# Performance work log

Hardware: AMD Instinct MI355X
Metric: run time of the kernel (lower is better)

The kernel has to match this reference:

```python
import jax, jax.numpy as jnp
import numpy as np

B, C, H, W = 8, 128, 64, 64   # batch, hidden_dim, spatial
CIN = 192                      # input_dim
N, K, R, DFF = 1, 4, 8, 512    # d_state, scan dirs, dt_rank=ceil(128/16), mlp hidden
EPS = 1e-5


def _conv1x1(t, w, b=None):
    y = jnp.einsum('bchw,oc->bohw', t, w)
    return y + b[None, :, None, None] if b is not None else y


def _ln_cf(t, g, bta):
    # LayerNorm over channel dim (channel_first)
    mu = t.mean(1, keepdims=True)
    var = ((t - mu) ** 2).mean(1, keepdims=True)
    return (t - mu) * jax.lax.rsqrt(var + EPS) * g[None, :, None, None] + bta[None, :, None, None]


def _forward(h, cz, cr, cq, x,
             in_proj_w, in_proj_b, ln1_g, ln1_b,
             ssm_in_w, conv_w, conv_b,
             x_proj_w, dt_w, dt_b, A_logs, Ds,
             outnorm_g, outnorm_b, out_proj_w,
             ln2_g, ln2_b, fc1_w, fc1_b, fc2_w, fc2_b,
             gate_w, gate_b):
    combined = jnp.concatenate([h, x], axis=1)          # [B, C+CIN, H, W]
    feat = _conv1x1(combined, in_proj_w, in_proj_b)     # [B, C, H, W]

    # ---- SS2D (v2_noz, channel_first) ----
    u = _conv1x1(_ln_cf(feat, ln1_g, ln1_b), ssm_in_w)  # in_proj (no bias)
    u = jax.lax.conv_general_dilated(u, conv_w, (1, 1), [(1, 1), (1, 1)],
                                     dimension_numbers=('NCHW', 'OIHW', 'NCHW'),
                                     feature_group_count=C)
    u = jax.nn.silu(u + conv_b[None, :, None, None])

    L = H * W
    x0 = u.reshape(B, C, L)
    x1 = u.transpose(0, 1, 3, 2).reshape(B, C, L)       # column-major scan
    xs = jnp.stack([x0, x1, x0[..., ::-1], x1[..., ::-1]], axis=1)  # [B,K,C,L]

    x_dbl = jnp.einsum('bkcl,kdc->bkdl', xs, x_proj_w)  # [B,K,R+2N,L]
    dts, Bs, Cs = jnp.split(x_dbl, [R, R + N], axis=2)
    delta = jax.nn.softplus(jnp.einsum('bkrl,kcr->bkcl', dts, dt_w) + dt_b[None, :, :, None])
    A = -jnp.exp(A_logs).reshape(K, C, N)
    D = Ds.reshape(K, C)

    dA = jnp.exp(delta[..., None] * A[None, :, :, None, :])                   # [B,K,C,L,N]
    dBu = (delta * xs)[..., None] * Bs.transpose(0, 1, 3, 2)[:, :, None, :, :]  # [B,K,C,L,N]

    def step(hst, inp):
        dA_t, dBu_t, C_t = inp
        hst = dA_t * hst + dBu_t                         # [B,K,C,N]
        return hst, jnp.einsum('bkcn,bkn->bkc', hst, C_t)

    init = jnp.zeros((B, K, C, N), u.dtype)
    _, ys = jax.lax.scan(step, init,
                         (dA.transpose(3, 0, 1, 2, 4),
                          dBu.transpose(3, 0, 1, 2, 4),
                          Cs.transpose(3, 0, 1, 2)))
    ys = ys.transpose(1, 2, 3, 0)                        # [B,K,C,L]
    ys = ys + D[None, :, :, None] * xs

    # cross-merge: undo flips and transposes, sum directions
    y = ys[:, 0] + ys[:, 2, :, ::-1]
    y_t = ys[:, 1] + ys[:, 3, :, ::-1]
    y = y + y_t.reshape(B, C, W, H).transpose(0, 1, 3, 2).reshape(B, C, L)
    y = y.reshape(B, C, H, W)
    y = _ln_cf(y, outnorm_g, outnorm_b)
    ssm_out = _conv1x1(y, out_proj_w)

    # ---- VSSBlock residuals (drop_path identity in eval) ----
    z = feat + ssm_out
    m = _conv1x1(_ln_cf(z, ln2_g, ln2_b), fc1_w, fc1_b)
    m = jax.nn.gelu(m, approximate=False)
    m = _conv1x1(m, fc2_w, fc2_b)
    z = z + m

    # ---- gated update ----
    g = jax.nn.sigmoid(_conv1x1(z, gate_w, gate_b))
    return g * z + (1.0 - g) * h


def setup_inputs() -> dict:
    key = jax.random.key(0)
    ks = jax.random.split(key, 20)
    rn = lambda i, shape, s=0.02: jax.random.normal(ks[i], shape, jnp.float32) * s
    return dict(
        h=jax.random.normal(ks[0], (B, C, H, W), jnp.float32),
        cz=jax.random.normal(ks[1], (B, C, H, W), jnp.float32),
        cr=jax.random.normal(ks[2], (B, C, H, W), jnp.float32),
        cq=jax.random.normal(ks[3], (B, C, H, W), jnp.float32),
        x=jax.random.normal(ks[4], (B, CIN, H, W), jnp.float32),
        in_proj_w=rn(5, (C, C + CIN)), in_proj_b=jnp.zeros(C, jnp.float32),
        ln1_g=jnp.ones(C, jnp.float32), ln1_b=jnp.zeros(C, jnp.float32),
        ssm_in_w=rn(6, (C, C)),
        conv_w=rn(7, (C, 1, 3, 3), 0.1), conv_b=jnp.zeros(C, jnp.float32),
        x_proj_w=rn(8, (K, R + 2 * N, C)),
        dt_w=rn(9, (K, C, R), 0.1), dt_b=rn(10, (K, C), 0.1),
        A_logs=jnp.zeros((K * C, N), jnp.float32),
        Ds=jnp.ones(K * C, jnp.float32),
        outnorm_g=jnp.ones(C, jnp.float32), outnorm_b=jnp.zeros(C, jnp.float32),
        out_proj_w=rn(11, (C, C)),
        ln2_g=jnp.ones(C, jnp.float32), ln2_b=jnp.zeros(C, jnp.float32),
        fc1_w=rn(12, (DFF, C)), fc1_b=jnp.zeros(DFF, jnp.float32),
        fc2_w=rn(13, (C, DFF)), fc2_b=jnp.zeros(C, jnp.float32),
        gate_w=rn(14, (C, C)), gate_b=jnp.zeros(C, jnp.float32),
    )


def reference(h, cz, cr, cq, x,
              in_proj_w, in_proj_b, ln1_g, ln1_b,
              ssm_in_w, conv_w, conv_b,
              x_proj_w, dt_w, dt_b, A_logs, Ds,
              outnorm_g, outnorm_b, out_proj_w,
              ln2_g, ln2_b, fc1_w, fc1_b, fc2_w, fc2_b,
              gate_w, gate_b):
    return _forward(h, cz, cr, cq, x,
                    in_proj_w, in_proj_b, ln1_g, ln1_b,
                    ssm_in_w, conv_w, conv_b,
                    x_proj_w, dt_w, dt_b, A_logs, Ds,
                    outnorm_g, outnorm_b, out_proj_w,
                    ln2_g, ln2_b, fc1_w, fc1_b, fc2_w, fc2_b,
                    gate_w, gate_b)
```

## Files before the change

### kernel.cpp

```cpp
#include <hip/hip_runtime.h>
#include <hip/hip_bf16.h>

constexpr int B_ = 8, C_ = 128, Hh = 64, Ww = 64, L_ = Hh * Ww;
constexpr int CIN_ = 192, K_ = 4, Rr = 8, DFF_ = 512;
constexpr long SZ1 = (long)B_ * C_ * L_;
constexpr float EPSf = 1e-5f;
constexpr float LOG2E = 1.44269504088896f;
constexpr float LN2f  = 0.693147180559945f;

#define DEVI __device__ __forceinline__

using s16x4 = __attribute__((ext_vector_type(4))) short;
using s16x8 = __attribute__((ext_vector_type(8))) short;
using f32x4 = __attribute__((ext_vector_type(4))) float;

DEVI float sigm(float x) { return 1.f / (1.f + __expf(-x)); }
DEVI float geluf(float x) { return 0.5f * x * (1.f + erff(x * 0.70710678118654752f)); }
DEVI float siluf(float x) { return x * sigm(x); }

DEVI unsigned short f2bf(float f) {
    unsigned u = __float_as_uint(f);
    u += 0x7fffu + ((u >> 16) & 1u);
    return (unsigned short)(u >> 16);
}
DEVI float bf2f(unsigned short u) { return __uint_as_float((unsigned)u << 16); }

DEVI int tadr(int pos) { return ((pos & 63) << 6) | (pos >> 6); }

template <int BN, bool ACC, bool BIAS, bool XGELU, bool SIG, bool GATE, bool SPLIT,
          bool XLN, bool LNOUT, bool XBF, bool OUTBF>
__global__ __launch_bounds__(256) void gemm_k(
    const float* __restrict__ W, const float* __restrict__ X1, long sX1,
    const float* __restrict__ X2, long sX2, int splitRow,
    const float* __restrict__ bias,
    const float* __restrict__ xmu, const float* __restrict__ xrs,
    const float* __restrict__ xg, const float* __restrict__ xbt,
    float* __restrict__ NOut, const float* __restrict__ og, const float* __restrict__ obt,
    float* __restrict__ Cp, long sC, int M, int N, int K)
{
    constexpr int NI = BN / 32;
    __shared__ unsigned short sA[128][40];
    __shared__ unsigned short sB[BN][40];
    const int tid = threadIdx.x;
    const int bn = blockIdx.x, bm = blockIdx.y, bz = blockIdx.z;
    const float* X1b = X1 + (XBF ? 0 : (long)bz * sX1);
    const unsigned short* X1u = XBF ? ((const unsigned short*)X1 + (long)bz * sX1) : nullptr;
    const float* X2b = (SPLIT || GATE) ? (X2 + (long)bz * sX2) : nullptr;
    float* Cb = Cp + (long)bz * sC;
    unsigned short* Cu = OUTBF ? ((unsigned short*)Cp + (long)bz * sC) : nullptr;
    const int n0 = bn * BN, m0 = bm * 128;

    const int l = tid & 63, w = tid >> 6;
    const int wm = w >> 1, wn = w & 1;
    const int lr = l & 15, lk = (l >> 4) * 8;

    const int awrow = tid >> 1, awk = (tid & 1) * 16;

    f32x4 acc[4][NI];
#pragma unroll
    for (int i = 0; i < 4; i++)
#pragma unroll
        for (int j = 0; j < NI; j++) acc[i][j] = (f32x4)0.f;

    for (int k0 = 0; k0 < K; k0 += 32) {
        {
            const float* wp = W + (long)(m0 + awrow) * K + k0 + awk;
            float4 f0 = *(const float4*)(wp + 0);
            float4 f1 = *(const float4*)(wp + 4);
            float4 f2 = *(const float4*)(wp + 8);
            float4 f3 = *(const float4*)(wp + 12);
            s16x8 v0, v1;
            v0[0]=f2bf(f0.x); v0[1]=f2bf(f0.y); v0[2]=f2bf(f0.z); v0[3]=f2bf(f0.w);
            v0[4]=f2bf(f1.x); v0[5]=f2bf(f1.y); v0[6]=f2bf(f1.z); v0[7]=f2bf(f1.w);
            v1[0]=f2bf(f2.x); v1[1]=f2bf(f2.y); v1[2]=f2bf(f2.z); v1[3]=f2bf(f2.w);
            v1[4]=f2bf(f3.x); v1[5]=f2bf(f3.y); v1[6]=f2bf(f3.z); v1[7]=f2bf(f3.w);
            *(s16x8*)&sA[awrow][awk] = v0;
            *(s16x8*)&sA[awrow][awk + 8] = v1;
        }
        if constexpr (BN == 128) {
            const int bnb = tid & 31, bkb = tid >> 5;
            const int krow = k0 + bkb * 4;
            const int colk = n0 + bnb * 4;
            float4 r0, r1, r2, r3;
            if constexpr (XBF) {
                ushort4 a0 = *(const ushort4*)(X1u + (long)krow * N + colk);
                ushort4 a1 = *(const ushort4*)(X1u + (long)(krow + 1) * N + colk);
                ushort4 a2 = *(const ushort4*)(X1u + (long)(krow + 2) * N + colk);
                ushort4 a3 = *(const ushort4*)(X1u + (long)(krow + 3) * N + colk);
                r0 = make_float4(bf2f(a0.x), bf2f(a0.y), bf2f(a0.z), bf2f(a0.w));
                r1 = make_float4(bf2f(a1.x), bf2f(a1.y), bf2f(a1.z), bf2f(a1.w));
                r2 = make_float4(bf2f(a2.x), bf2f(a2.y), bf2f(a2.z), bf2f(a2.w));
                r3 = make_float4(bf2f(a3.x), bf2f(a3.y), bf2f(a3.z), bf2f(a3.w));
            } else {
                const float* xp;
                if (SPLIT && krow >= splitRow)
                    xp = X2b + (long)(krow - splitRow) * N + colk;
                else
                    xp = X1b + (long)krow * N + colk;
                r0 = *(const float4*)(xp + 0 * (long)N);
                r1 = *(const float4*)(xp + 1 * (long)N);
                r2 = *(const float4*)(xp + 2 * (long)N);
                r3 = *(const float4*)(xp + 3 * (long)N);
            }
            if (XGELU) {
                r0.x=geluf(r0.x); r0.y=geluf(r0.y); r0.z=geluf(r0.z); r0.w=geluf(r0.w);
                r1.x=geluf(r1.x); r1.y=geluf(r1.y); r1.z=geluf(r1.z); r1.w=geluf(r1.w);
                r2.x=geluf(r2.x); r2.y=geluf(r2.y); r2.z=geluf(r2.z); r2.w=geluf(r2.w);
                r3.x=geluf(r3.x); r3.y=geluf(r3.y); r3.z=geluf(r3.z); r3.w=geluf(r3.w);
            }
            const float* p0 = (const float*)&r0;
            const float* p1 = (const float*)&r1;
            const float* p2 = (const float*)&r2;
            const float* p3 = (const float*)&r3;
#pragma unroll
            for (int c = 0; c < 4; c++) {
                s16x4 v;
                v[0] = f2bf(p0[c]); v[1] = f2bf(p1[c]);
                v[2] = f2bf(p2[c]); v[3] = f2bf(p3[c]);
                *(s16x4*)&sB[bnb * 4 + c][bkb * 4] = v;
            }
        } else {
            const int bnb = tid & 15, bkb = tid >> 4;
            const int krow = k0 + bkb * 2;
            const int col0 = n0 + bnb * 4;
            float4 r0, r1;
            if constexpr (XBF) {
                ushort4 a0 = *(const ushort4*)(X1u + (long)krow * N + col0);
                ushort4 a1 = *(const ushort4*)(X1u + (long)(krow + 1) * N + col0);
                r0 = make_float4(bf2f(a0.x), bf2f(a0.y), bf2f(a0.z), bf2f(a0.w));
                r1 = make_float4(bf2f(a1.x), bf2f(a1.y), bf2f(a1.z), bf2f(a1.w));
            } else {
                const float* xpa;
                const float* xpb;
                if (SPLIT && krow >= splitRow)
                    xpa = X2b + (long)(krow - splitRow) * N + col0;
                else
                    xpa = X1b + (long)krow * N + col0;
                if (SPLIT && (krow + 1) >= splitRow)
                    xpb = X2b + (long)(krow + 1 - splitRow) * N + col0;
                else
                    xpb = X1b + (long)(krow + 1) * N + col0;
                r0 = *(const float4*)xpa;
                r1 = *(const float4*)xpb;
                if (XLN) {
                    float4 m4 = *(const float4*)(xmu + (long)bz * N + col0);
                    float4 s4 = *(const float4*)(xrs + (long)bz * N + col0);
                    float ga = xg[krow], be = xbt[krow];
                    r0.x=(r0.x-m4.x)*s4.x*ga+be; r0.y=(r0.y-m4.y)*s4.y*ga+be;
                    r0.z=(r0.z-m4.z)*s4.z*ga+be; r0.w=(r0.w-m4.w)*s4.w*ga+be;
                    ga = xg[krow + 1]; be = xbt[krow + 1];
                    r1.x=(r1.x-m4.x)*s4.x*ga+be; r1.y=(r1.y-m4.y)*s4.y*ga+be;
                    r1.z=(r1.z-m4.z)*s4.z*ga+be; r1.w=(r1.w-m4.w)*s4.w*ga+be;
                }
            }
            if (XGELU) {
                r0.x=geluf(r0.x); r0.y=geluf(r0.y); r0.z=geluf(r0.z); r0.w=geluf(r0.w);
                r1.x=geluf(r1.x); r1.y=geluf(r1.y); r1.z=geluf(r1.z); r1.w=geluf(r1.w);
            }
            const float* p0 = (const float*)&r0;
            const float* p1 = (const float*)&r1;
#pragma unroll
            for (int c = 0; c < 4; c++) {
                unsigned v = (unsigned)f2bf(p0[c]) | ((unsigned)f2bf(p1[c]) << 16);
                *(unsigned*)&sB[bnb * 4 + c][bkb * 2] = v;
            }
        }
        __syncthreads();
        s16x8 af[4], bf[NI];
#pragma unroll
        for (int mi = 0; mi < 4; mi++) af[mi] = *(const s16x8*)&sA[wm * 64 + mi * 16 + lr][lk];
#pragma unroll
        for (int ni = 0; ni < NI; ni++) bf[ni] = *(const s16x8*)&sB[wn * (BN / 2) + ni * 16 + lr][lk];
#pragma unroll
        for (int mi = 0; mi < 4; mi++)
#pragma unroll
            for (int ni = 0; ni < NI; ni++)
                acc[mi][ni] = __builtin_amdgcn_mfma_f32_16x16x32_bf16(af[mi], bf[ni], acc[mi][ni], 0, 0, 0);
        __syncthreads();
    }

    float ps[NI], pq[NI];
    if (LNOUT) {
#pragma unroll
        for (int ni = 0; ni < NI; ni++) { ps[ni] = 0.f; pq[ni] = 0.f; }
    }
#pragma unroll
    for (int mi = 0; mi < 4; mi++) {
#pragma unroll
        for (int r = 0; r < 4; r++) {
            const int row = m0 + wm * 64 + mi * 16 + (l >> 4) * 4 + r;
            const float bv = BIAS ? bias[row] : 0.f;
#pragma unroll
            for (int ni = 0; ni < NI; ni++) {
                const int col = n0 + wn * (BN / 2) + ni * 16 + lr;
                float v = acc[mi][ni][r] + bv;
                if constexpr (OUTBF) {
                    Cu[(long)row * N + col] = f2bf(v);
                } else {
                    float* cp = Cb + (long)row * N + col;
                    if (ACC) v += *cp;
                    if (SIG) v = sigm(v);
                    if (GATE) {
                        v = sigm(v);
                        float zv = X1b[(long)row * N + col];
                        float hv = X2b[(long)row * N + col];
                        v = hv + v * (zv - hv);
                    }
                    *cp = v;
                }
                if (LNOUT) {
                    acc[mi][ni][r] = v;
                    ps[ni] += v; pq[ni] += v * v;
                }
            }
        }
    }
    if constexpr (LNOUT) {
        __shared__ float redS[2][2][NI][16];
        __shared__ float redQ[2][2][NI][16];
        __shared__ float muL[BN], rsL[BN];
#pragma unroll
        for (int ni = 0; ni < NI; ni++) {
            ps[ni] += __shfl_xor(ps[ni], 16, 64);
            ps[ni] += __shfl_xor(ps[ni], 32, 64);
            pq[ni] += __shfl_xor(pq[ni], 16, 64);
            pq[ni] += __shfl_xor(pq[ni], 32, 64);
        }
        if (l < 16) {
#pragma unroll
            for (int ni = 0; ni < NI; ni++) {
                redS[wm][wn][ni][l] = ps[ni];
                redQ[wm][wn][ni][l] = pq[ni];
            }
        }
        __syncthreads();
        if (tid < BN) {
            const int cc = tid;
            const int wn2 = cc >> 5, rem = cc & 31;
            const int ni2 = rem >> 4, lr2 = rem & 15;
            float s = redS[0][wn2][ni2][lr2] + redS[1][wn2][ni2][lr2];
            float q = redQ[0][wn2][ni2][lr2] + redQ[1][wn2][ni2][lr2];
            float mu = s * (1.f / 128.f);
            float var = q * (1.f / 128.f) - mu * mu;
            muL[cc] = mu;
            rsL[cc] = rsqrtf(var + EPSf);
        }
        __syncthreads();
        unsigned short* Nb = (unsigned short*)NOut + (long)bz * sC;
#pragma unroll
        for (int mi = 0; mi < 4; mi++) {
#pragma unroll
            for (int r = 0; r < 4; r++) {
                const int row = m0 + wm * 64 + mi * 16 + (l >> 4) * 4 + r;
                const float gg = og[row], bb = obt[row];
#pragma unroll
                for (int ni = 0; ni < NI; ni++) {
                    const int cc = wn * (BN / 2) + ni * 16 + lr;
                    const int col = n0 + cc;
                    float v = acc[mi][ni][r];
                    Nb[(long)row * N + col] = f2bf((v - muL[cc]) * rsL[cc] * gg + bb);
                }
            }
        }
    }
}

__global__ __launch_bounds__(256) void ln_stats_k(const float* __restrict__ in,
                                                  float* __restrict__ mu,
                                                  float* __restrict__ rs)
{
    __shared__ float s1[4][64], s2[4][64];
    const int tid = threadIdx.x;
    const int p = tid & 63, q = tid >> 6;
    const long posg = (long)blockIdx.x * 64 + p;
    const int b = (int)(posg / L_);
    const int pp = (int)(posg % L_);
    const float* base = in + ((long)b * C_ + q * 32) * L_ + pp;
    float s = 0.f, sq = 0.f;
#pragma unroll
    for (int i = 0; i < 32; i++) {
        float t = base[(long)i * L_];
        s += t; sq += t * t;
    }
    s1[q][p] = s; s2[q][p] = sq;
    __syncthreads();
    if (q == 0) {
        float ts = s1[0][p] + s1[1][p] + s1[2][p] + s1[3][p];
        float tq = s2[0][p] + s2[1][p] + s2[2][p] + s2[3][p];
        float m = ts * (1.f / 128.f);
        float var = tq * (1.f / 128.f) - m * m;
        mu[posg] = m;
        rs[posg] = rsqrtf(var + EPSf);
    }
}

__global__ __launch_bounds__(256) void dwconvT_k(const unsigned short* __restrict__ in,
                                                 const float* __restrict__ wts,
                                                 const float* __restrict__ bias,
                                                 float* __restrict__ uo,
                                                 float* __restrict__ uTo)
{
    __shared__ float t[64][65];
    const long plane = blockIdx.x;
    const int c = (int)(plane & 127);
    const int tid = threadIdx.x;
    const unsigned short* src = in + plane * (long)L_;
#pragma unroll
    for (int ii = 0; ii < 16; ii++) {
        int idx = tid + ii * 256;
        t[idx >> 6][idx & 63] = bf2f(src[idx]);
    }
    float kw[9];
#pragma unroll
    for (int q = 0; q < 9; q++) kw[q] = wts[c * 9 + q];
    const float bc = bias[c];
    __syncthreads();
    float r[16];
#pragma unroll
    for (int ii = 0; ii < 16; ii++) {
        int idx = tid + ii * 256;
        int h = idx >> 6, w2 = idx & 63;
        float acc = bc;
#pragma unroll
        for (int dh = -1; dh <= 1; dh++) {
            int hh = h + dh;
            if ((unsigned)hh >= 64u) continue;
#pragma unroll
            for (int dw = -1; dw <= 1; dw++) {
                int ww2 = w2 + dw;
                if ((unsigned)ww2 >= 64u) continue;
                acc += t[hh][ww2] * kw[(dh + 1) * 3 + (dw + 1)];
            }
        }
        r[ii] = siluf(acc);
    }
    __syncthreads();
    float* ud = uo + plane * (long)L_;
#pragma unroll
    for (int ii = 0; ii < 16; ii++) {
        int idx = tid + ii * 256;
        t[idx >> 6][idx & 63] = r[ii];
        ud[idx] = r[ii];
    }
    __syncthreads();
    float* utd = uTo + plane * (long)L_;
#pragma unroll
    for (int ii = 0; ii < 16; ii++) {
        int idx = tid + ii * 256;
        utd[idx] = t[idx & 63][idx >> 6];
    }
}

template <bool ADD>
__global__ __launch_bounds__(256) void transp_k(const float* __restrict__ src,
                                                float* __restrict__ dst)
{
    __shared__ float t[64][65];
    const long plane = blockIdx.x;
    const float* s = src + plane * (long)L_;
    float* d = dst + plane * (long)L_;
    const int tid = threadIdx.x;
#pragma unroll
    for (int i = 0; i < 16; i++) {
        int idx = tid + i * 256;
        t[idx >> 6][idx & 63] = s[idx];
    }
    __syncthreads();
#pragma unroll
    for (int i = 0; i < 16; i++) {
        int idx = tid + i * 256;
        int r = idx >> 6, cc = idx & 63;
        float val = t[cc][r];
        if (ADD) d[idx] += val; else d[idx] = val;
    }
}

__global__ __launch_bounds__(256) void xdbl2_k(const float* __restrict__ u,
                                               const float* __restrict__ uT,
                                               const float* __restrict__ xw,
                                               float* __restrict__ out)
{
    __shared__ float wsm[2][16][132];
    const int pair = blockIdx.y, b = blockIdx.z;
    const int tid = threadIdx.x;
#pragma unroll
    for (int i = 0; i < 8; i++) {
        int idx = tid * 8 + i;
        wsm[0][idx >> 7][idx & 127] = xw[pair * 2048 + idx];
        wsm[1][idx >> 7][idx & 127] = xw[(pair + 2) * 2048 + idx];
    }
    __syncthreads();
    const int dg = (tid & 3) * 4;
    const int lo = tid >> 2;
    const int pos = blockIdx.x * 64 + lo;
    const float* usrc = (pair ? uT : u) + (long)b * C_ * L_ + pos;
    float a0[4] = {0.f, 0.f, 0.f, 0.f};
    float a1[4] = {0.f, 0.f, 0.f, 0.f};
#pragma unroll 4
    for (int c = 0; c < C_; c++) {
        float uc = usrc[(long)c * L_];
#pragma unroll
        for (int j = 0; j < 4; j++) {
            a0[j] += wsm[0][dg + j][c] * uc;
            a1[j] += wsm[1][dg + j][c] * uc;
        }
    }
    const long baseA = ((long)(b * K_ + pair) * L_) << 4;
    const long baseB = ((long)(b * K_ + pair + 2) * L_) << 4;
    const int s  = tadr(pos);
    const int s2 = tadr(L_ - 1 - pos);
    *(float4*)(out + baseA + ((long)s  << 4) + dg) = make_float4(a0[0], a0[1], a0[2], a0[3]);
    *(float4*)(out + baseB + ((long)s2 << 4) + dg) = make_float4(a1[0], a1[1], a1[2], a1[3]);
}

__global__ __launch_bounds__(256) void scan_ph1L_k(const float* __restrict__ xdbl,
                                                   const float* __restrict__ u,
                                                   const float* __restrict__ uT,
                                                   const float* __restrict__ dtw,
                                                   const float* __restrict__ dtb,
                                                   const float* __restrict__ alogs,
                                                   float* __restrict__ st)
{
    __shared__ float xtf[2][32][16];
    __shared__ float xtb[2][32][16];
    const int bid = blockIdx.x;
    const int jj = bid & 63, kh = (bid >> 6) & 1, b = bid >> 7;
    const int t = threadIdx.x;
    const int kf = kh, kb = kh + 2;
    const float* xf = xdbl + ((long)(b * 4 + kf) << 16);
    const float* xb = xdbl + ((long)(b * 4 + kb) << 16);
    {
        const int q = t & 3, i = (t >> 2) & 31, j2 = t >> 7;
        const int jf = 2 * jj + j2, jB = 127 - jf;
        const int sf = (((jf & 1) * 32 + i) << 6) | (jf >> 1);
        const int sb = (((jB & 1) * 32 + i) << 6) | (jB >> 1);
        *(float4*)&xtf[j2][i][q * 4] = *(const float4*)(xf + (long)sf * 16 + q * 4);
        *(float4*)&xtb[j2][i][q * 4] = *(const float4*)(xb + (long)sb * 16 + q * 4);
    }
    const int c = t & 127, jh = t >> 7;
    const int jf = 2 * jj + jh, jB = 127 - jf;
    const float* uplane = (kh ? uT : u) + (long)(b * 128 + c) * L_;
    float ur[32];
    {
        const float* up = uplane + jf * 32;
#pragma unroll
        for (int q = 0; q < 8; q++) *(float4*)&ur[q * 4] = *(const float4*)(up + q * 4);
    }
    __syncthreads();
    {
        float dw[8];
#pragma unroll
        for (int r = 0; r < 8; r++) dw[r] = dtw[((kf * 128 + c) << 3) + r];
        const float db = dtb[kf * 128 + c];
        float An[4];
#pragma unroll
        for (int n = 0; n < 4; n++) An[n] = -__expf(alogs[((kf * 128 + c) << 2) + n]);
        float P0 = 1.f, P1 = 1.f, P2 = 1.f, P3 = 1.f;
        float S0 = 0.f, S1 = 0.f, S2 = 0.f, S3 = 0.f;
#pragma unroll
        for (int i = 0; i < 32; i++) {
            float4 x0 = *(const float4*)&xtf[jh][i][0];
            float4 x1 = *(const float4*)&xtf[jh][i][4];
            float4 xs = *(const float4*)&xtf[jh][i][8];
            float z = db + x0.x*dw[0] + x0.y*dw[1] + x0.z*dw[2] + x0.w*dw[3]
                         + x1.x*dw[4] + x1.y*dw[5] + x1.z*dw[6] + x1.w*dw[7];
            float wv = (z > 15.f) ? z * LOG2E : log2f(1.f + __expf(z));
            float dl = wv * LN2f;
            float du = dl * ur[i];
            float e;
            e = exp2f(wv * An[0]); S0 = e * S0 + du * xs.x; P0 *= e;
            e = exp2f(wv * An[1]); S1 = e * S1 + du * xs.y; P1 *= e;
            e = exp2f(wv * An[2]); S2 = e * S2 + du * xs.z; P2 *= e;
            e = exp2f(wv * An[3]); S3 = e * S3 + du * xs.w; P3 *= e;
        }
        float* o = st + ((long)((b * 4 + kf) * 128 + c) << 10) + (jf << 3);
        *(float4*)o = make_float4(P0, P1, P2, P3);
        *(float4*)(o + 4) = make_float4(S0, S1, S2, S3);
    }
    {
        float dw[8];
#pragma unroll
        for (int r = 0; r < 8; r++) dw[r] = dtw[((kb * 128 + c) << 3) + r];
        const float db = dtb[kb * 128 + c];
        float An[4];
#pragma unroll
        for (int n = 0; n < 4; n++) An[n] = -__expf(alogs[((kb * 128 + c) << 2) + n]);
        float P0 = 1.f, P1 = 1.f, P2 = 1.f, P3 = 1.f;
        float S0 = 0.f, S1 = 0.f, S2 = 0.f, S3 = 0.f;
#pragma unroll
        for (int i = 0; i < 32; i++) {
            float4 x0 = *(const float4*)&xtb[jh][i][0];
            float4 x1 = *(const float4*)&xtb[jh][i][4];
            float4 xs = *(const float4*)&xtb[jh][i][8];
            float z = db + x0.x*dw[0] + x0.y*dw[1] + x0.z*dw[2] + x0.w*dw[3]
                         + x1.x*dw[4] + x1.y*dw[5] + x1.z*dw[6] + x1.w*dw[7];
            float wv = (z > 15.f) ? z * LOG2E : log2f(1.f + __expf(z));
            float dl = wv * LN2f;
            float du = dl * ur[31 - i];
            float e;
            e = exp2f(wv * An[0]); S0 = e * S0 + du * xs.x; P0 *= e;
            e = exp2f(wv * An[1]); S1 = e * S1 + du * xs.y; P1 *= e;
            e = exp2f(wv * An[2]); S2 = e * S2 + du * xs.z; P2 *= e;
            e = exp2f(wv * An[3]); S3 = e * S3 + du * xs.w; P3 *= e;
        }
        float* o = st + ((long)((b * 4 + kb) * 128 + c) << 10) + (jB << 3);
        *(float4*)o = make_float4(P0, P1, P2, P3);
        *(float4*)(o + 4) = make_float4(S0, S1, S2, S3);
    }
}

__global__ __launch_bounds__(256) void scan_mid_k(float* __restrict__ st)
{
    const long t = (long)blockIdx.x * 256 + threadIdx.x;
    const long chain = t >> 6;
    const int ln = (int)(t & 63);
    float* base = st + (chain << 10) + (ln << 4);
    float4 Pa = *(float4*)(base + 0);
    float4 Sa = *(float4*)(base + 4);
    float4 Pb = *(float4*)(base + 8);
    float4 Sb = *(float4*)(base + 12);
    float4 P, S;
    P.x = Pb.x * Pa.x; P.y = Pb.y * Pa.y; P.z = Pb.z * Pa.z; P.w = Pb.w * Pa.w;
    S.x = Sb.x + Pb.x * Sa.x; S.y = Sb.y + Pb.y * Sa.y;
    S.z = Sb.z + Pb.z * Sa.z; S.w = Sb.w + Pb.w * Sa.w;
#pragma unroll
    for (int d = 1; d < 64; d <<= 1) {
        float4 Pu, Su;
        Pu.x = __shfl_up(P.x, d, 64); Pu.y = __shfl_up(P.y, d, 64);
        Pu.z = __shfl_up(P.z, d, 64); Pu.w = __shfl_up(P.w, d, 64);
        Su.x = __shfl_up(S.x, d, 64); Su.y = __shfl_up(S.y, d, 64);
        Su.z = __shfl_up(S.z, d, 64); Su.w = __shfl_up(S.w, d, 64);
        if (ln >= d) {
            S.x += P.x * Su.x; S.y += P.y * Su.y;
            S.z += P.z * Su.z; S.w += P.w * Su.w;
            P.x *= Pu.x; P.y *= Pu.y; P.z *= Pu.z; P.w *= Pu.w;
        }
    }
    float4 E;
    E.x = __shfl_up(S.x, 1, 64); E.y = __shfl_up(S.y, 1, 64);
    E.z = __shfl_up(S.z, 1, 64); E.w = __shfl_up(S.w, 1, 64);
    if (ln == 0) { E.x = 0.f; E.y = 0.f; E.z = 0.f; E.w = 0.f; }
    float4 E1;
    E1.x = Sa.x + Pa.x * E.x; E1.y = Sa.y + Pa.y * E.y;
    E1.z = Sa.z + Pa.z * E.z; E1.w = Sa.w + Pa.w * E.w;
    *(float4*)(base + 4)  = E;
    *(float4*)(base + 12) = E1;
}

__global__ __launch_bounds__(256) void scan_ph2L_k(const float* __restrict__ xdbl,
                                                   const float* __restrict__ u,
                                                   const float* __restrict__ uT,
                                                   const float* __restrict__ dtw,
                                                   const float* __restrict__ dtb,
                                                   const float* __restrict__ alogs,
                                                   const float* __restrict__ Dsp,
                                                   const float* __restrict__ st,
                                                   float* __restrict__ Y0,
                                                   float* __restrict__ Yt)
{
    __shared__ float xtf[2][32][16];
    __shared__ float xtb[2][32][16];
    __shared__ float yt[128][65];
    const int bid = blockIdx.x;
    const int jj = bid & 63, kh = (bid >> 6) & 1, b = bid >> 7;
    const int t = threadIdx.x;
    const int kf = kh, kb = kh + 2;
    const float* xf = xdbl + ((long)(b * 4 + kf) << 16);
    const float* xb = xdbl + ((long)(b * 4 + kb) << 16);
    {
        const int q = t & 3, i = (t >> 2) & 31, j2 = t >> 7;
        const int jf = 2 * jj + j2, jB = 127 - jf;
        const int sf = (((jf & 1) * 32 + i) << 6) | (jf >> 1);
        const int sb = (((jB & 1) * 32 + i) << 6) | (jB >> 1);
        *(float4*)&xtf[j2][i][q * 4] = *(const float4*)(xf + (long)sf * 16 + q * 4);
        *(float4*)&xtb[j2][i][q * 4] = *(const float4*)(xb + (long)sb * 16 + q * 4);
    }
    const int c = t & 127, jh = t >> 7;
    const int jf = 2 * jj + jh, jB = 127 - jf;
    const float* uplane = (kh ? uT : u) + (long)(b * 128 + c) * L_;
    float ur[32];
    {
        const float* up = uplane + jf * 32;
#pragma unroll
        for (int q = 0; q < 8; q++) *(float4*)&ur[q * 4] = *(const float4*)(up + q * 4);
    }
    __syncthreads();
    {
        float dw[8];
#pragma unroll
        for (int r = 0; r < 8; r++) dw[r] = dtw[((kf * 128 + c) << 3) + r];
        const float db = dtb[kf * 128 + c];
        float An[4];
#pragma unroll
        for (int n = 0; n < 4; n++) An[n] = -__expf(alogs[((kf * 128 + c) << 2) + n]);
        const float Dc = Dsp[kf * 128 + c];
        float4 H = *(const float4*)(st + ((long)((b * 4 + kf) * 128 + c) << 10) + (jf << 3) + 4);
        float h0 = H.x, h1 = H.y, h2 = H.z, h3 = H.w;
#pragma unroll
        for (int i = 0; i < 32; i++) {
            float4 x0 = *(const float4*)&xtf[jh][i][0];
            float4 x1 = *(const float4*)&xtf[jh][i][4];
            float4 xs = *(const float4*)&xtf[jh][i][8];
            float4 xc = *(const float4*)&xtf[jh][i][12];
            float z = db + x0.x*dw[0] + x0.y*dw[1] + x0.z*dw[2] + x0.w*dw[3]
                         + x1.x*dw[4] + x1.y*dw[5] + x1.z*dw[6] + x1.w*dw[7];
            float wv = (z > 15.f) ? z * LOG2E : log2f(1.f + __expf(z));
            float dl = wv * LN2f;
            float du = dl * ur[i];
            float e;
            e = exp2f(wv * An[0]); h0 = e * h0 + du * xs.x;
            e = exp2f(wv * An[1]); h1 = e * h1 + du * xs.y;
            e = exp2f(wv * An[2]); h2 = e * h2 + du * xs.z;
            e = exp2f(wv * An[3]); h3 = e * h3 + du * xs.w;
            yt[c][jh * 32 + i] = h0 * xc.x + h1 * xc.y + h2 * xc.z + h3 * xc.w + Dc * ur[i];
        }
    }
    {
        float dw[8];
#pragma unroll
        for (int r = 0; r < 8; r++) dw[r] = dtw[((kb * 128 + c) << 3) + r];
        const float db = dtb[kb * 128 + c];
        float An[4];
#pragma unroll
        for (int n = 0; n < 4; n++) An[n] = -__expf(alogs[((kb * 128 + c) << 2) + n]);
        const float Dc = Dsp[kb * 128 + c];
        float4 H = *(const float4*)(st + ((long)((b * 4 + kb) * 128 + c) << 10) + (jB << 3) + 4);
        float h0 = H.x, h1 = H.y, h2 = H.z, h3 = H.w;
#pragma unroll
        for (int i = 0; i < 32; i++) {
            float4 x0 = *(const float4*)&xtb[jh][i][0];
            float4 x1 = *(const float4*)&xtb[jh][i][4];
            float4 xs = *(const float4*)&xtb[jh][i][8];
            float4 xc = *(const float4*)&xtb[jh][i][12];
            float z = db + x0.x*dw[0] + x0.y*dw[1] + x0.z*dw[2] + x0.w*dw[3]
                         + x1.x*dw[4] + x1.y*dw[5] + x1.z*dw[6] + x1.w*dw[7];
            float wv = (z > 15.f) ? z * LOG2E : log2f(1.f + __expf(z));
            float dl = wv * LN2f;
            float uv = ur[31 - i];
            float du = dl * uv;
            float e;
            e = exp2f(wv * An[0]); h0 = e * h0 + du * xs.x;
            e = exp2f(wv * An[1]); h1 = e * h1 + du * xs.y;
            e = exp2f(wv * An[2]); h2 = e * h2 + du * xs.z;
            e = exp2f(wv * An[3]); h3 = e * h3 + du * xs.w;
            yt[c][jh * 32 + 31 - i] += h0 * xc.x + h1 * xc.y + h2 * xc.z + h3 * xc.w + Dc * uv;
        }
    }
    __syncthreads();
    float* ydst = (kh ? Yt : Y0) + (long)(b * 128) * L_ + jj * 64;
    const int pos = t & 63, cg = t >> 6;
#pragma unroll
    for (int rep = 0; rep < 32; rep++) {
        const int c2 = cg + rep * 4;
        ydst[(long)c2 * L_ + pos] = yt[c2][pos];
    }
}

extern "C" void kernel_launch(void* const* d_in, const int* in_sizes, int n_in,
                              void* d_out, int out_size, void* d_ws, size_t ws_size,
                              hipStream_t stream)
{
    const float* h_in      = (const float*)d_in[0];
    const float* x_in      = (const float*)d_in[4];
    const float* in_proj_w = (const float*)d_in[5];
    const float* in_proj_b = (const float*)d_in[6];
    const float* ln1_g     = (const float*)d_in[7];
    const float* ln1_b     = (const float*)d_in[8];
    const float* ssm_in_w  = (const float*)d_in[9];
    const float* conv_w    = (const float*)d_in[10];
    const float* conv_b    = (const float*)d_in[11];
    const float* x_proj_w  = (const float*)d_in[12];
    const float* dt_w      = (const float*)d_in[13];
    const float* dt_b      = (const float*)d_in[14];
    const float* A_logs    = (const float*)d_in[15];
    const float* Dsp       = (const float*)d_in[16];
    const float* outnorm_g = (const float*)d_in[17];
    const float* outnorm_b = (const float*)d_in[18];
    const float* out_proj_w= (const float*)d_in[19];
    const float* ln2_g     = (const float*)d_in[20];
    const float* ln2_b     = (const float*)d_in[21];
    const float* fc1_w     = (const float*)d_in[22];
    const float* fc1_b     = (const float*)d_in[23];
    const float* fc2_w     = (const float*)d_in[24];
    const float* fc2_b     = (const float*)d_in[25];
    const float* gate_w    = (const float*)d_in[26];
    const float* gate_b    = (const float*)d_in[27];

    float* ws   = (float*)d_ws;
    float* fz   = ws;
    float* ubuf = ws + SZ1;
    float* tbuf = ws + 2 * SZ1;
    float* ybuf = ws + 3 * SZ1;
    float* xdbl = ws + 4 * SZ1;
    float* stbf = ws + 4 * SZ1 + 2097152;
    float* muB  = stbf;
    float* rsB  = stbf + 32768;
    float* mbuf = ubuf;
    float* gbuf = (float*)d_out;

    const dim3 blk(256);
    const long sBC = (long)C_ * L_;
    const long sX  = (long)CIN_ * L_;
    const long sM  = (long)DFF_ * L_;

    gemm_k<64, false, true, false, false, false, true, false, true, false, false>
        <<<dim3(64, 1, 8), blk, 0, stream>>>(
        in_proj_w, h_in, sBC, x_in, sX, 128, in_proj_b,
        nullptr, nullptr, nullptr, nullptr, ybuf, ln1_g, ln1_b,
        fz, sBC, 128, L_, 320);
    gemm_k<64, false, false, false, false, false, false, false, false, true, true>
        <<<dim3(64, 1, 8), blk, 0, stream>>>(
        ssm_in_w, ybuf, sBC, nullptr, 0, 1 << 30, nullptr,
        nullptr, nullptr, nullptr, nullptr, nullptr, nullptr, nullptr,
        tbuf, sBC, 128, L_, 128);
    dwconvT_k<<<dim3(1024), blk, 0, stream>>>((const unsigned short*)tbuf,
                                              conv_w, conv_b, ubuf, ybuf);
    xdbl2_k<<<dim3(64, 2, 8), blk, 0, stream>>>(ubuf, ybuf, x_proj_w, xdbl);
    scan_ph1L_k<<<dim3(1024), blk, 0, stream>>>(xdbl, ubuf, ybuf, dt_w, dt_b, A_logs, stbf);
    scan_mid_k<<<dim3(1024), blk, 0, stream>>>(stbf);
    scan_ph2L_k<<<dim3(1024), blk, 0, stream>>>(xdbl, ubuf, ybuf, dt_w, dt_b,
                                                A_logs, Dsp, stbf, tbuf, gbuf);
    transp_k<true><<<dim3(1024), blk, 0, stream>>>(gbuf, tbuf);
    ln_stats_k<<<dim3(512), blk, 0, stream>>>(tbuf, muB, rsB);
    gemm_k<64, true, false, false, false, false, false, true, true, false, false>
        <<<dim3(64, 1, 8), blk, 0, stream>>>(
        out_proj_w, tbuf, sBC, nullptr, 0, 1 << 30, nullptr,
        muB, rsB, outnorm_g, outnorm_b, gbuf, ln2_g, ln2_b,
        fz, sBC, 128, L_, 128);
    gemm_k<128, false, true, false, false, false, false, false, false, true, true>
        <<<dim3(32, 4, 8), blk, 0, stream>>>(
        fc1_w, gbuf, sBC, nullptr, 0, 1 << 30, fc1_b,
        nullptr, nullptr, nullptr, nullptr, nullptr, nullptr, nullptr,
        mbuf, sM, 512, L_, 128);
    gemm_k<64, true, true, true, false, false, false, false, false, true, false>
        <<<dim3(64, 1, 8), blk, 0, stream>>>(
        fc2_w, mbuf, sM, nullptr, 0, 1 << 30, fc2_b,
        nullptr, nullptr, nullptr, nullptr, nullptr, nullptr, nullptr,
        fz, sBC, 128, L_, 512);
    gemm_k<64, false, true, false, false, true, false, false, false, false, false>
        <<<dim3(64, 1, 8), blk, 0, stream>>>(
        gate_w, fz, sBC, h_in, sBC, 1 << 30, gate_b,
        nullptr, nullptr, nullptr, nullptr, nullptr, nullptr, nullptr,
        (float*)d_out, sBC, 128, L_, 128);
}
```

Before: 236.6 us.

## Store SSM intermediates (u, uT, scan outputs) in bf16 to halve traffic

The depthwise conv outputs, their transposed copy, the scan outputs and the transposed sum are now stored as bf16 instead of fp32. The consumers (xdbl projection, both scan phases, the transpose-add, the LN stats and the out_proj GEMM via its bf16-input path) convert on load. The GEMM's LayerNorm-on-input step is moved so it also applies to the bf16 input path. This halves memory traffic across several bandwidth-bound kernels, at the cost of lower precision, including bf16 rounding of the forward/backward scan accumulation held in shared memory.

```diff
diff --git a/kernel.cpp b/kernel.cpp
--- a/kernel.cpp
+++ b/kernel.cpp
@@ -142,16 +142,16 @@
                     xpb = X1b + (long)(krow + 1) * N + col0;
                 r0 = *(const float4*)xpa;
                 r1 = *(const float4*)xpb;
-                if (XLN) {
-                    float4 m4 = *(const float4*)(xmu + (long)bz * N + col0);
-                    float4 s4 = *(const float4*)(xrs + (long)bz * N + col0);
-                    float ga = xg[krow], be = xbt[krow];
-                    r0.x=(r0.x-m4.x)*s4.x*ga+be; r0.y=(r0.y-m4.y)*s4.y*ga+be;
-                    r0.z=(r0.z-m4.z)*s4.z*ga+be; r0.w=(r0.w-m4.w)*s4.w*ga+be;
-                    ga = xg[krow + 1]; be = xbt[krow + 1];
-                    r1.x=(r1.x-m4.x)*s4.x*ga+be; r1.y=(r1.y-m4.y)*s4.y*ga+be;
-                    r1.z=(r1.z-m4.z)*s4.z*ga+be; r1.w=(r1.w-m4.w)*s4.w*ga+be;
-                }
+            }
+            if (XLN) {
+                float4 m4 = *(const float4*)(xmu + (long)bz * N + col0);
+                float4 s4 = *(const float4*)(xrs + (long)bz * N + col0);
+                float ga = xg[krow], be = xbt[krow];
+                r0.x=(r0.x-m4.x)*s4.x*ga+be; r0.y=(r0.y-m4.y)*s4.y*ga+be;
+                r0.z=(r0.z-m4.z)*s4.z*ga+be; r0.w=(r0.w-m4.w)*s4.w*ga+be;
+                ga = xg[krow + 1]; be = xbt[krow + 1];
+                r1.x=(r1.x-m4.x)*s4.x*ga+be; r1.y=(r1.y-m4.y)*s4.y*ga+be;
+                r1.z=(r1.z-m4.z)*s4.z*ga+be; r1.w=(r1.w-m4.w)*s4.w*ga+be;
             }
             if (XGELU) {
                 r0.x=geluf(r0.x); r0.y=geluf(r0.y); r0.z=geluf(r0.z); r0.w=geluf(r0.w);
@@ -265,7 +265,7 @@
     }
 }
 
-__global__ __launch_bounds__(256) void ln_stats_k(const float* __restrict__ in,
+__global__ __launch_bounds__(256) void ln_stats_k(const unsigned short* __restrict__ in,
                                                   float* __restrict__ mu,
                                                   float* __restrict__ rs)
 {
@@ -275,11 +275,11 @@
     const long posg = (long)blockIdx.x * 64 + p;
     const int b = (int)(posg / L_);
     const int pp = (int)(posg % L_);
-    const float* base = in + ((long)b * C_ + q * 32) * L_ + pp;
+    const unsigned short* base = in + ((long)b * C_ + q * 32) * L_ + pp;
     float s = 0.f, sq = 0.f;
 #pragma unroll
     for (int i = 0; i < 32; i++) {
-        float t = base[(long)i * L_];
+        float t = bf2f(base[(long)i * L_]);
         s += t; sq += t * t;
     }
     s1[q][p] = s; s2[q][p] = sq;
@@ -297,8 +297,8 @@
 __global__ __launch_bounds__(256) void dwconvT_k(const unsigned short* __restrict__ in,
                                                  const float* __restrict__ wts,
                                                  const float* __restrict__ bias,
-                                                 float* __restrict__ uo,
-                                                 float* __restrict__ uTo)
+                                                 unsigned short* __restrict__ uo,
+                                                 unsigned short* __restrict__ uTo)
 {
     __shared__ float t[64][65];
     const long plane = blockIdx.x;
@@ -335,48 +335,47 @@
         r[ii] = siluf(acc);
     }
     __syncthreads();
-    float* ud = uo + plane * (long)L_;
+    unsigned short* ud = uo + plane * (long)L_;
 #pragma unroll
     for (int ii = 0; ii < 16; ii++) {
         int idx = tid + ii * 256;
         t[idx >> 6][idx & 63] = r[ii];
-        ud[idx] = r[ii];
-    }
-    __syncthreads();
-    float* utd = uTo + plane * (long)L_;
+        ud[idx] = f2bf(r[ii]);
+    }
+    __syncthreads();
+    unsigned short* utd = uTo + plane * (long)L_;
 #pragma unroll
     for (int ii = 0; ii < 16; ii++) {
         int idx = tid + ii * 256;
-        utd[idx] = t[idx & 63][idx >> 6];
-    }
-}
-
-template <bool ADD>
-__global__ __launch_bounds__(256) void transp_k(const float* __restrict__ src,
-                                                float* __restrict__ dst)
+        utd[idx] = f2bf(t[idx & 63][idx >> 6]);
+    }
+}
+
+__global__ __launch_bounds__(256) void transpb_k(const unsigned short* __restrict__ src,
+                                                 unsigned short* __restrict__ dst)
 {
     __shared__ float t[64][65];
     const long plane = blockIdx.x;
-    const float* s = src + plane * (long)L_;
-    float* d = dst + plane * (long)L_;
+    const unsigned short* s = src + plane * (long)L_;
+    unsigned short* d = dst + plane * (long)L_;
     const int tid = threadIdx.x;
 #pragma unroll
     for (int i = 0; i < 16; i++) {
         int idx = tid + i * 256;
-        t[idx >> 6][idx & 63] = s[idx];
+        t[idx >> 6][idx & 63] = bf2f(s[idx]);
     }
     __syncthreads();
 #pragma unroll
     for (int i = 0; i < 16; i++) {
         int idx = tid + i * 256;
         int r = idx >> 6, cc = idx & 63;
-        float val = t[cc][r];
-        if (ADD) d[idx] += val; else d[idx] = val;
-    }
-}
-
-__global__ __launch_bounds__(256) void xdbl2_k(const float* __restrict__ u,
-                                               const float* __restrict__ uT,
+        float val = t[cc][r] + bf2f(d[idx]);
+        d[idx] = f2bf(val);
+    }
+}
+
+__global__ __launch_bounds__(256) void xdbl2_k(const unsigned short* __restrict__ u,
+                                               const unsigned short* __restrict__ uT,
                                                const float* __restrict__ xw,
                                                float* __restrict__ out)
 {
@@ -393,12 +392,12 @@
     const int dg = (tid & 3) * 4;
     const int lo = tid >> 2;
     const int pos = blockIdx.x * 64 + lo;
-    const float* usrc = (pair ? uT : u) + (long)b * C_ * L_ + pos;
+    const unsigned short* usrc = (pair ? uT : u) + (long)b * C_ * L_ + pos;
     float a0[4] = {0.f, 0.f, 0.f, 0.f};
     float a1[4] = {0.f, 0.f, 0.f, 0.f};
 #pragma unroll 4
     for (int c = 0; c < C_; c++) {
-        float uc = usrc[(long)c * L_];
+        float uc = bf2f(usrc[(long)c * L_]);
 #pragma unroll
         for (int j = 0; j < 4; j++) {
             a0[j] += wsm[0][dg + j][c] * uc;
@@ -414,8 +413,8 @@
 }
 
 __global__ __launch_bounds__(256) void scan_ph1L_k(const float* __restrict__ xdbl,
-                                                   const float* __restrict__ u,
-                                                   const float* __restrict__ uT,
+                                                   const unsigned short* __restrict__ u,
+                                                   const unsigned short* __restrict__ uT,
                                                    const float* __restrict__ dtw,
                                                    const float* __restrict__ dtb,
                                                    const float* __restrict__ alogs,
@@ -439,12 +438,16 @@
     }
     const int c = t & 127, jh = t >> 7;
     const int jf = 2 * jj + jh, jB = 127 - jf;
-    const float* uplane = (kh ? uT : u) + (long)(b * 128 + c) * L_;
+    const unsigned short* uplane = (kh ? uT : u) + (long)(b * 128 + c) * L_;
     float ur[32];
     {
-        const float* up = uplane + jf * 32;
-#pragma unroll
-        for (int q = 0; q < 8; q++) *(float4*)&ur[q * 4] = *(const float4*)(up + q * 4);
+        const unsigned short* up = uplane + jf * 32;
+#pragma unroll
+        for (int q = 0; q < 8; q++) {
+            ushort4 a = *(const ushort4*)(up + q * 4);
+            ur[q * 4 + 0] = bf2f(a.x); ur[q * 4 + 1] = bf2f(a.y);
+            ur[q * 4 + 2] = bf2f(a.z); ur[q * 4 + 3] = bf2f(a.w);
+        }
     }
     __syncthreads();
     {
@@ -548,19 +551,19 @@
 }
 
 __global__ __launch_bounds__(256) void scan_ph2L_k(const float* __restrict__ xdbl,
-                                                   const float* __restrict__ u,
-                                                   const float* __restrict__ uT,
+                                                   const unsigned short* __restrict__ u,
+                                                   const unsigned short* __restrict__ uT,
                                                    const float* __restrict__ dtw,
                                                    const float* __restrict__ dtb,
                                                    const float* __restrict__ alogs,
                                                    const float* __restrict__ Dsp,
                                                    const float* __restrict__ st,
-                                                   float* __restrict__ Y0,
-                                                   float* __restrict__ Yt)
+                                                   unsigned short* __restrict__ Y0,
+                                                   unsigned short* __restrict__ Yt)
 {
     __shared__ float xtf[2][32][16];
     __shared__ float xtb[2][32][16];
-    __shared__ float yt[128][65];
+    __shared__ unsigned short yt[128][66];
     const int bid = blockIdx.x;
     const int jj = bid & 63, kh = (bid >> 6) & 1, b = bid >> 7;
     const int t = threadIdx.x;
@@ -577,12 +580,16 @@
     }
     const int c = t & 127, jh = t >> 7;
     const int jf = 2 * jj + jh, jB = 127 - jf;
-    const float* uplane = (kh ? uT : u) + (long)(b * 128 + c) * L_;
+    const unsigned short* uplane = (kh ? uT : u) + (long)(b * 128 + c) * L_;
     float ur[32];
     {
-        const float* up = uplane + jf * 32;
-#pragma unroll
-        for (int q = 0; q < 8; q++) *(float4*)&ur[q * 4] = *(const float4*)(up + q * 4);
+        const unsigned short* up = uplane + jf * 32;
+#pragma unroll
+        for (int q = 0; q < 8; q++) {
+            ushort4 a = *(const ushort4*)(up + q * 4);
+            ur[q * 4 + 0] = bf2f(a.x); ur[q * 4 + 1] = bf2f(a.y);
+            ur[q * 4 + 2] = bf2f(a.z); ur[q * 4 + 3] = bf2f(a.w);
+        }
     }
     __syncthreads();
     {
@@ -612,7 +619,7 @@
             e = exp2f(wv * An[1]); h1 = e * h1 + du * xs.y;
             e = exp2f(wv * An[2]); h2 = e * h2 + du * xs.z;
             e = exp2f(wv * An[3]); h3 = e * h3 + du * xs.w;
-            yt[c][jh * 32 + i] = h0 * xc.x + h1 * xc.y + h2 * xc.z + h3 * xc.w + Dc * ur[i];
+            yt[c][jh * 32 + i] = f2bf(h0 * xc.x + h1 * xc.y + h2 * xc.z + h3 * xc.w + Dc * ur[i]);
         }
     }
     {
@@ -643,11 +650,13 @@
             e = exp2f(wv * An[1]); h1 = e * h1 + du * xs.y;
             e = exp2f(wv * An[2]); h2 = e * h2 + du * xs.z;
             e = exp2f(wv * An[3]); h3 = e * h3 + du * xs.w;
-            yt[c][jh * 32 + 31 - i] += h0 * xc.x + h1 * xc.y + h2 * xc.z + h3 * xc.w + Dc * uv;
-        }
-    }
-    __syncthreads();
-    float* ydst = (kh ? Yt : Y0) + (long)(b * 128) * L_ + jj * 64;
+            const int slot = jh * 32 + 31 - i;
+            float prev = bf2f(yt[c][slot]);
+            yt[c][slot] = f2bf(prev + h0 * xc.x + h1 * xc.y + h2 * xc.z + h3 * xc.w + Dc * uv);
+        }
+    }
+    __syncthreads();
+    unsigned short* ydst = (kh ? Yt : Y0) + (long)(b * 128) * L_ + jj * 64;
     const int pos = t & 63, cg = t >> 6;
 #pragma unroll
     for (int rep = 0; rep < 32; rep++) {
@@ -698,6 +707,12 @@
     float* mbuf = ubuf;
     float* gbuf = (float*)d_out;
 
+    unsigned short* u_u  = (unsigned short*)ubuf;
+    unsigned short* u0_u = (unsigned short*)tbuf;
+    unsigned short* uT_u = (unsigned short*)ybuf;
+    unsigned short* y0_u = (unsigned short*)tbuf;
+    unsigned short* yt_u = (unsigned short*)gbuf;
+
     const dim3 blk(256);
     const long sBC = (long)C_ * L_;
     const long sX  = (long)CIN_ * L_;
@@ -713,16 +728,15 @@
         ssm_in_w, ybuf, sBC, nullptr, 0, 1 << 30, nullptr,
         nullptr, nullptr, nullptr, nullptr, nullptr, nullptr, nullptr,
         tbuf, sBC, 128, L_, 128);
-    dwconvT_k<<<dim3(1024), blk, 0, stream>>>((const unsigned short*)tbuf,
-                                              conv_w, conv_b, ubuf, ybuf);
-    xdbl2_k<<<dim3(64, 2, 8), blk, 0, stream>>>(ubuf, ybuf, x_proj_w, xdbl);
-    scan_ph1L_k<<<dim3(1024), blk, 0, stream>>>(xdbl, ubuf, ybuf, dt_w, dt_b, A_logs, stbf);
+    dwconvT_k<<<dim3(1024), blk, 0, stream>>>(u0_u, conv_w, conv_b, u_u, uT_u);
+    xdbl2_k<<<dim3(64, 2, 8), blk, 0, stream>>>(u_u, uT_u, x_proj_w, xdbl);
+    scan_ph1L_k<<<dim3(1024), blk, 0, stream>>>(xdbl, u_u, uT_u, dt_w, dt_b, A_logs, stbf);
     scan_mid_k<<<dim3(1024), blk, 0, stream>>>(stbf);
-    scan_ph2L_k<<<dim3(1024), blk, 0, stream>>>(xdbl, ubuf, ybuf, dt_w, dt_b,
-                                                A_logs, Dsp, stbf, tbuf, gbuf);
-    transp_k<true><<<dim3(1024), blk, 0, stream>>>(gbuf, tbuf);
-    ln_stats_k<<<dim3(512), blk, 0, stream>>>(tbuf, muB, rsB);
-    gemm_k<64, true, false, false, false, false, false, true, true, false, false>
+    scan_ph2L_k<<<dim3(1024), blk, 0, stream>>>(xdbl, u_u, uT_u, dt_w, dt_b,
+                                                A_logs, Dsp, stbf, y0_u, yt_u);
+    transpb_k<<<dim3(1024), blk, 0, stream>>>(yt_u, y0_u);
+    ln_stats_k<<<dim3(512), blk, 0, stream>>>(y0_u, muB, rsB);
+    gemm_k<64, true, false, false, false, false, false, true, true, true, false>
         <<<dim3(64, 1, 8), blk, 0, stream>>>(
         out_proj_w, tbuf, sBC, nullptr, 0, 1 << 30, nullptr,
         muB, rsB, outnorm_g, outnorm_b, gbuf, ln2_g, ln2_b,
```

Result: no change. 234.9 us (-0.7%).
